# Kernel optimization log

Hardware: AMD Instinct MI355X
Metric: run time of the kernel (lower is better)

Reference implementation:

```python
import jax, jax.numpy as jnp
import numpy as np

EPS = 1e-12  # matches torch F.normalize eps default scale behavior (1e-12)

def _l2_normalize(x):
    n = jnp.sqrt(jnp.sum(x * x, axis=-1, keepdims=True))
    return x / jnp.maximum(n, EPS)

def setup_inputs() -> dict:
    key = jax.random.key(0)
    k1, k2 = jax.random.split(key)
    B, K, D = 32768, 4096, 1024
    context_repr = jax.random.normal(k1, (B, D), dtype=jnp.float32)
    # matches nn.init.normal_(std=0.02)
    cluster_centers = 0.02 * jax.random.normal(k2, (K, D), dtype=jnp.float32)
    return {"context_repr": context_repr, "cluster_centers": cluster_centers}

def reference(context_repr, cluster_centers):
    # L2-normalize rows of both
    x = _l2_normalize(context_repr)        # [B, D]
    c = _l2_normalize(cluster_centers)     # [K, D]
    x2 = jnp.sum(x * x, axis=-1, keepdims=True)          # [B, 1]
    c2 = jnp.sum(c * c, axis=-1)[None, :]                # [1, K]
    d2 = x2 + c2 - 2.0 * jnp.einsum('bd,kd->bk', x, c)   # [B, K]
    hard = jnp.argmin(d2, axis=-1)                       # [B]
    # Gather the UN-normalized learnable centers (as in the torch code)
    cluster_embedding = cluster_centers[hard]            # [B, D]
    return cluster_embedding
```

## Files before the change

### kernel.cpp

```cpp
#include <hip/hip_runtime.h>
#include <stdint.h>

#define B_ROWS 32768
#define K_CENT 4096
#define D_DIM  1024
#define EPS_CAND 5e-4f

typedef unsigned short u16;
typedef __attribute__((ext_vector_type(8))) __bf16 bf16x8;
typedef __attribute__((ext_vector_type(4))) float f32x4;

__device__ inline u16 f32_to_bf16(float f) {
    unsigned u = __float_as_uint(f);
    u += 0x7FFFu + ((u >> 16) & 1u);
    return (u16)(u >> 16);
}
__device__ inline float bf16_to_f32(u16 h) {
    return __uint_as_float(((unsigned)h) << 16);
}
__device__ inline unsigned ord_of_f32(float f) {
    unsigned u = __float_as_uint(f);
    return (u & 0x80000000u) ? ~u : (u | 0x80000000u);
}
__device__ inline float f32_of_ord(unsigned o) {
    unsigned u = (o & 0x80000000u) ? (o & 0x7fffffffu) : ~o;
    return __uint_as_float(u);
}

__global__ __launch_bounds__(256) void prep_rows(
    const float* __restrict__ src, u16* __restrict__ hi, u16* __restrict__ lo,
    float* __restrict__ sq, float* __restrict__ den)
{
    __shared__ double sm[4];
    const int row = blockIdx.x, tid = threadIdx.x;
    const float4 v = reinterpret_cast<const float4*>(src + (size_t)row * D_DIM)[tid];
    double ss = (double)v.x * v.x + (double)v.y * v.y
              + (double)v.z * v.z + (double)v.w * v.w;
#pragma unroll
    for (int m = 1; m < 64; m <<= 1) ss += __shfl_xor(ss, m, 64);
    if ((tid & 63) == 0) sm[tid >> 6] = ss;
    __syncthreads();
    const double tot = sm[0] + sm[1] + sm[2] + sm[3];
    const float d = fmaxf(sqrtf((float)tot), 1e-12f);
    const float n0 = v.x / d, n1 = v.y / d, n2 = v.z / d, n3 = v.w / d;

    ushort4 h, l;
    h.x = f32_to_bf16(n0); l.x = f32_to_bf16(n0 - bf16_to_f32(h.x));
    h.y = f32_to_bf16(n1); l.y = f32_to_bf16(n1 - bf16_to_f32(h.y));
    h.z = f32_to_bf16(n2); l.z = f32_to_bf16(n2 - bf16_to_f32(h.z));
    h.w = f32_to_bf16(n3); l.w = f32_to_bf16(n3 - bf16_to_f32(h.w));
    reinterpret_cast<ushort4*>(hi + (size_t)row * D_DIM)[tid] = h;
    reinterpret_cast<ushort4*>(lo + (size_t)row * D_DIM)[tid] = l;

    double s2 = (double)n0 * n0 + (double)n1 * n1
              + (double)n2 * n2 + (double)n3 * n3;
#pragma unroll
    for (int m = 1; m < 64; m <<= 1) s2 += __shfl_xor(s2, m, 64);
    __syncthreads();
    if ((tid & 63) == 0) sm[tid >> 6] = s2;
    __syncthreads();
    if (tid == 0) {
        sq[row] = (float)(sm[0] + sm[1] + sm[2] + sm[3]);
        den[row] = d;
    }
}

#define BM 256
#define BN 128
#define BK 32
#define NT (D_DIM / BK)
#define REG_U16 4096
#define TILE_U16 (6 * REG_U16)

__global__ __launch_bounds__(512, 2) void gemm_cand(
    const u16* __restrict__ Ahi, const u16* __restrict__ Alo,
    const u16* __restrict__ Bhi, const u16* __restrict__ Blo,
    const float* __restrict__ c2, unsigned long long* __restrict__ cand)
{
    __shared__ u16 lds[3 * TILE_U16];

    const int tid = threadIdx.x, lane = tid & 63, w = tid >> 6;
    const int wm = w >> 1, wn = w & 1;
    const int fr = lane & 15, fc = lane >> 4;

    const int flat = blockIdx.x;
    const int swz = (flat & 7) * 512 + (flat >> 3);
    int bx = swz & 31;
    const int by = swz >> 5;
    if (by & 1) bx = 31 - bx;
    const size_t arow0 = (size_t)by * BM;
    const size_t brow0 = (size_t)bx * BN;

    const int p = w * 64 + lane;
    const int srow = p >> 2;
    const int scc = (p & 3) ^ ((srow >> 1) & 3);
    const u16* gsrc[6];
    gsrc[0] = Ahi + (arow0 + srow) * D_DIM + scc * 8;
    gsrc[1] = Ahi + (arow0 + 128 + srow) * D_DIM + scc * 8;
    gsrc[2] = Alo + (arow0 + srow) * D_DIM + scc * 8;
    gsrc[3] = Alo + (arow0 + 128 + srow) * D_DIM + scc * 8;
    gsrc[4] = Bhi + (brow0 + srow) * D_DIM + scc * 8;
    gsrc[5] = Blo + (brow0 + srow) * D_DIM + scc * 8;
    const int ldw = w * 512;

    int offA[4], offB[4];
#pragma unroll
    for (int i = 0; i < 4; ++i) {
        const int ar = wm * 64 + i * 16 + fr;
        const int rg = ar >> 7, rr = ar & 127;
        offA[i] = rg * REG_U16 + rr * 32 + ((fc ^ ((rr >> 1) & 3)) * 8);
        const int br = wn * 64 + i * 16 + fr;
        offB[i] = br * 32 + ((fc ^ ((br >> 1) & 3)) * 8);
    }

    f32x4 acc[4][4] = {};

#define STAGE3(t, J0)                                                         \
    do {                                                                      \
        const int _base = ((t) % 3) * TILE_U16;                               \
        const int _k = (t) * BK;                                              \
        _Pragma("unroll")                                                     \
        for (int _j = (J0); _j < (J0) + 3; ++_j)                              \
            __builtin_amdgcn_global_load_lds(                                 \
                (const __attribute__((address_space(1))) void*)(gsrc[_j] + _k), \
                (__attribute__((address_space(3))) void*)(lds + _base + _j * REG_U16 + ldw), \
                16, 0, 0);                                                    \
    } while (0)

    STAGE3(0, 0); STAGE3(0, 3);
    STAGE3(1, 0); STAGE3(1, 3);
    asm volatile("s_waitcnt vmcnt(6)" ::: "memory");
    __builtin_amdgcn_s_barrier();

    for (int t = 0; t < NT; ++t) {
        const int cb = (t % 3) * TILE_U16;

        bf16x8 bhf[4], blf[4], ah0[2], al0[2];
#pragma unroll
        for (int n = 0; n < 4; ++n) {
            bhf[n] = *reinterpret_cast<const bf16x8*>(lds + cb + 4 * REG_U16 + offB[n]);
            blf[n] = *reinterpret_cast<const bf16x8*>(lds + cb + 5 * REG_U16 + offB[n]);
        }
#pragma unroll
        for (int i = 0; i < 2; ++i) {
            ah0[i] = *reinterpret_cast<const bf16x8*>(lds + cb + offA[i]);
            al0[i] = *reinterpret_cast<const bf16x8*>(lds + cb + 2 * REG_U16 + offA[i]);
        }
        if (t + 2 < NT) STAGE3(t + 2, 0);
        __builtin_amdgcn_sched_barrier(0);
        __builtin_amdgcn_s_barrier();
        __builtin_amdgcn_s_setprio(1);
#pragma unroll
        for (int i = 0; i < 2; ++i)
#pragma unroll
            for (int n = 0; n < 4; ++n)
                acc[i][n] = __builtin_amdgcn_mfma_f32_16x16x32_bf16(ah0[i], bhf[n], acc[i][n], 0, 0, 0);
#pragma unroll
        for (int i = 0; i < 2; ++i)
#pragma unroll
            for (int n = 0; n < 4; ++n)
                acc[i][n] = __builtin_amdgcn_mfma_f32_16x16x32_bf16(ah0[i], blf[n], acc[i][n], 0, 0, 0);
#pragma unroll
        for (int i = 0; i < 2; ++i)
#pragma unroll
            for (int n = 0; n < 4; ++n)
                acc[i][n] = __builtin_amdgcn_mfma_f32_16x16x32_bf16(al0[i], bhf[n], acc[i][n], 0, 0, 0);
        __builtin_amdgcn_s_setprio(0);
        __builtin_amdgcn_s_barrier();

        bf16x8 ah1[2], al1[2];
#pragma unroll
        for (int i = 0; i < 2; ++i) {
            ah1[i] = *reinterpret_cast<const bf16x8*>(lds + cb + offA[2 + i]);
            al1[i] = *reinterpret_cast<const bf16x8*>(lds + cb + 2 * REG_U16 + offA[2 + i]);
        }
        if (t + 2 < NT) STAGE3(t + 2, 3);
        __builtin_amdgcn_sched_barrier(0);
        __builtin_amdgcn_s_barrier();
        __builtin_amdgcn_s_setprio(1);
#pragma unroll
        for (int i = 0; i < 2; ++i)
#pragma unroll
            for (int n = 0; n < 4; ++n)
                acc[2 + i][n] = __builtin_amdgcn_mfma_f32_16x16x32_bf16(ah1[i], bhf[n], acc[2 + i][n], 0, 0, 0);
#pragma unroll
        for (int i = 0; i < 2; ++i)
#pragma unroll
            for (int n = 0; n < 4; ++n)
                acc[2 + i][n] = __builtin_amdgcn_mfma_f32_16x16x32_bf16(ah1[i], blf[n], acc[2 + i][n], 0, 0, 0);
#pragma unroll
        for (int i = 0; i < 2; ++i)
#pragma unroll
            for (int n = 0; n < 4; ++n)
                acc[2 + i][n] = __builtin_amdgcn_mfma_f32_16x16x32_bf16(al1[i], bhf[n], acc[2 + i][n], 0, 0, 0);
        __builtin_amdgcn_s_setprio(0);

        if (t < NT - 2)       asm volatile("s_waitcnt vmcnt(6)" ::: "memory");
        else if (t == NT - 2) asm volatile("s_waitcnt vmcnt(0)" ::: "memory");
        if (t < NT - 1) __builtin_amdgcn_s_barrier();
    }
#undef STAGE3

    const int group = bx * 2 + wn;
    float c2v[4];
#pragma unroll
    for (int n = 0; n < 4; ++n)
        c2v[n] = c2[brow0 + wn * 64 + n * 16 + fr];

#pragma unroll
    for (int mi = 0; mi < 4; ++mi) {
#pragma unroll
        for (int r = 0; r < 4; ++r) {
            unsigned long long bk = ~0ull;
#pragma unroll
            for (int ni = 0; ni < 4; ++ni) {
                const float d2a = c2v[ni] - 2.0f * acc[mi][ni][r];
                const unsigned col = (unsigned)(brow0 + wn * 64 + ni * 16 + fr);
                const unsigned long long key =
                    ((unsigned long long)ord_of_f32(d2a) << 32) | col;
                if (key < bk) bk = key;
            }
#pragma unroll
            for (int ms = 1; ms < 16; ms <<= 1) {
                const unsigned long long o = __shfl_xor(bk, ms, 64);
                if (o < bk) bk = o;
            }
            if (fr == 0) {
                const size_t grow = arow0 + wm * 64 + mi * 16 + fc * 4 + r;
                cand[grow * 64 + group] = bk;
            }
        }
    }
}

__global__ __launch_bounds__(256) void finalize(
    const unsigned long long* __restrict__ cand,
    const float* __restrict__ X, const float* __restrict__ C,
    const float* __restrict__ denx, const float* __restrict__ denc,
    const float* __restrict__ x2, const float* __restrict__ c2,
    float* __restrict__ out)
{
    const int w = threadIdx.x >> 6, lane = threadIdx.x & 63;
    const size_t row = (size_t)blockIdx.x * 4 + w;

    const unsigned long long v = cand[row * 64 + lane];
    unsigned long long m = v;
#pragma unroll
    for (int ms = 1; ms < 64; ms <<= 1) {
        const unsigned long long o = __shfl_xor(m, ms, 64);
        if (o < m) m = o;
    }
    const float fmin = f32_of_ord((unsigned)(m >> 32));
    const bool is_cand = f32_of_ord((unsigned)(v >> 32)) <= fmin + EPS_CAND;
    const unsigned long long ball = __ballot(is_cand);

    unsigned win;
    if (__popcll(ball) == 1) {
        win = (unsigned)(m & 0xffffffffu);
    } else {
        const float dxr = denx[row];
        const float x2r = x2[row];
        float xv[16];
#pragma unroll
        for (int j = 0; j < 16; ++j)
            xv[j] = X[row * D_DIM + j * 64 + lane] / dxr;

        float bestd2 = __uint_as_float(0x7f800000u);
        unsigned bwin = 0xffffffffu;
        unsigned long long bb = ball;
        while (bb) {
            const int l = __ffsll((unsigned long long)bb) - 1;
            bb &= bb - 1;
            const unsigned col = (unsigned)(__shfl(v, l, 64) & 0xffffffffu);
            const float dcr = denc[col];
            double s = 0.0;
#pragma unroll
            for (int j = 0; j < 16; ++j) {
                const float cv = C[(size_t)col * D_DIM + j * 64 + lane] / dcr;
                s = fma((double)xv[j], (double)cv, s);
            }
#pragma unroll
            for (int ms = 1; ms < 64; ms <<= 1) s += __shfl_xor(s, ms, 64);
            const float dotf = (float)s;
            const float d2 = (x2r + c2[col]) - 2.0f * dotf;
            if (d2 < bestd2 || (d2 == bestd2 && col < bwin)) {
                bestd2 = d2; bwin = col;
            }
        }
        win = bwin;
    }

    const float4* s4 = reinterpret_cast<const float4*>(C + (size_t)win * D_DIM);
    float4* d4 = reinterpret_cast<float4*>(out + row * D_DIM);
#pragma unroll
    for (int t = 0; t < 4; ++t) d4[t * 64 + lane] = s4[t * 64 + lane];
}

extern "C" void kernel_launch(void* const* d_in, const int* in_sizes, int n_in,
                              void* d_out, int out_size, void* d_ws, size_t ws_size,
                              hipStream_t stream)
{
    (void)in_sizes; (void)n_in; (void)out_size; (void)ws_size;
    const float* X = (const float*)d_in[0];
    const float* C = (const float*)d_in[1];
    float* out = (float*)d_out;

    char* ws = (char*)d_ws;
    u16* Ahi = (u16*)ws;
    u16* Alo = Ahi + (size_t)B_ROWS * D_DIM;
    u16* Bhi = Alo + (size_t)B_ROWS * D_DIM;
    u16* Blo = Bhi + (size_t)K_CENT * D_DIM;
    unsigned long long* cand =
        (unsigned long long*)(Blo + (size_t)K_CENT * D_DIM);
    float* c2   = (float*)(cand + (size_t)B_ROWS * 64);
    float* x2   = c2 + K_CENT;
    float* denx = x2 + B_ROWS;
    float* denc = denx + B_ROWS;

    prep_rows<<<B_ROWS, 256, 0, stream>>>(X, Ahi, Alo, x2, denx);
    prep_rows<<<K_CENT, 256, 0, stream>>>(C, Bhi, Blo, c2, denc);
    gemm_cand<<<(B_ROWS / BM) * (K_CENT / BN), 512, 0, stream>>>(
        Ahi, Alo, Bhi, Blo, c2, cand);
    finalize<<<B_ROWS / 4, 256, 0, stream>>>(
        cand, X, C, denx, denc, x2, c2, out);
}
```

Measured before the change: 1.060 ms.

## Enlarge GEMM tile to 256x256 and stream split-bf16 terms as K-phases

Widens the candidate GEMM block tile from 256x128 to 256x256 with 8 waves laid out 2x4, so each wave holds an 8x4 accumulator array. The three hi/lo product terms are no longer computed as separate MFMA groups inside each K step. Instead the K loop runs 48 steps over a concatenated K axis of hi*hi, lo*hi and hi*lo segments, selected by the tile index. The pipeline also moves from triple to double buffering with BK=64. The aim is more MFMA work per loaded byte and fewer separate fragment loads, at the cost of more accumulator registers and a shallower prefetch depth.

```diff
diff --git a/kernel.cpp b/kernel.cpp
--- a/kernel.cpp
+++ b/kernel.cpp
@@ -25,6 +25,11 @@
 __device__ inline float f32_of_ord(unsigned o) {
     unsigned u = (o & 0x80000000u) ? (o & 0x7fffffffu) : ~o;
     return __uint_as_float(u);
+}
+__device__ inline void gload_lds16(const u16* g, u16* l) {
+    __builtin_amdgcn_global_load_lds(
+        (const __attribute__((address_space(1))) void*)g,
+        (__attribute__((address_space(3))) void*)l, 16, 0, 0);
 }
 
 __global__ __launch_bounds__(256) void prep_rows(
@@ -66,149 +71,175 @@
 }
 
 #define BM 256
-#define BN 128
-#define BK 32
-#define NT (D_DIM / BK)
-#define REG_U16 4096
-#define TILE_U16 (6 * REG_U16)
+#define BN 256
+#define BK 64
+#define NT 48
+#define AREG 8192
+#define BOFF_U16 16384
+#define BUF_U16 32768
 
 __global__ __launch_bounds__(512, 2) void gemm_cand(
     const u16* __restrict__ Ahi, const u16* __restrict__ Alo,
     const u16* __restrict__ Bhi, const u16* __restrict__ Blo,
     const float* __restrict__ c2, unsigned long long* __restrict__ cand)
 {
-    __shared__ u16 lds[3 * TILE_U16];
+    __shared__ u16 lds[2 * BUF_U16];
 
     const int tid = threadIdx.x, lane = tid & 63, w = tid >> 6;
-    const int wm = w >> 1, wn = w & 1;
+    const int wm = w >> 2, wn = w & 3;
     const int fr = lane & 15, fc = lane >> 4;
 
     const int flat = blockIdx.x;
-    const int swz = (flat & 7) * 512 + (flat >> 3);
-    int bx = swz & 31;
-    const int by = swz >> 5;
-    if (by & 1) bx = 31 - bx;
+    const int swz = (flat & 7) * 256 + (flat >> 3);
+    int bx = swz & 15;
+    const int by = swz >> 4;
+    if (by & 1) bx = 15 - bx;
     const size_t arow0 = (size_t)by * BM;
     const size_t brow0 = (size_t)bx * BN;
 
-    const int p = w * 64 + lane;
-    const int srow = p >> 2;
-    const int scc = (p & 3) ^ ((srow >> 1) & 3);
-    const u16* gsrc[6];
-    gsrc[0] = Ahi + (arow0 + srow) * D_DIM + scc * 8;
-    gsrc[1] = Ahi + (arow0 + 128 + srow) * D_DIM + scc * 8;
-    gsrc[2] = Alo + (arow0 + srow) * D_DIM + scc * 8;
-    gsrc[3] = Alo + (arow0 + 128 + srow) * D_DIM + scc * 8;
-    gsrc[4] = Bhi + (brow0 + srow) * D_DIM + scc * 8;
-    gsrc[5] = Blo + (brow0 + srow) * D_DIM + scc * 8;
-    const int ldw = w * 512;
-
-    int offA[4], offB[4];
-#pragma unroll
-    for (int i = 0; i < 4; ++i) {
-        const int ar = wm * 64 + i * 16 + fr;
-        const int rg = ar >> 7, rr = ar & 127;
-        offA[i] = rg * REG_U16 + rr * 32 + ((fc ^ ((rr >> 1) & 3)) * 8);
-        const int br = wn * 64 + i * 16 + fr;
-        offB[i] = br * 32 + ((fc ^ ((br >> 1) & 3)) * 8);
-    }
-
-    f32x4 acc[4][4] = {};
-
-#define STAGE3(t, J0)                                                         \
-    do {                                                                      \
-        const int _base = ((t) % 3) * TILE_U16;                               \
-        const int _k = (t) * BK;                                              \
-        _Pragma("unroll")                                                     \
-        for (int _j = (J0); _j < (J0) + 3; ++_j)                              \
-            __builtin_amdgcn_global_load_lds(                                 \
-                (const __attribute__((address_space(1))) void*)(gsrc[_j] + _k), \
-                (__attribute__((address_space(3))) void*)(lds + _base + _j * REG_U16 + ldw), \
-                16, 0, 0);                                                    \
-    } while (0)
-
-    STAGE3(0, 0); STAGE3(0, 3);
-    STAGE3(1, 0); STAGE3(1, 3);
-    asm volatile("s_waitcnt vmcnt(6)" ::: "memory");
+    const int prow = tid >> 2, pch = tid & 3;
+    const int lc = pch ^ ((prow >> 1) & 3);
+    const size_t lane0 = (size_t)prow * D_DIM + lc * 8;
+    const size_t lane1 = (size_t)(prow + 128) * D_DIM + lc * 8;
+    const int dst0 = tid * 8, dst1 = tid * 8 + 4096;
+    const size_t abase = arow0 * D_DIM;
+    const size_t bbase = brow0 * D_DIM;
+
+#define STAGE_A(tn, jj) do {                                                  \
+    const u16* s_ = ((((tn) >> 4) == 1) ? Alo : Ahi) + abase                  \
+                    + ((size_t)((tn) & 15)) * BK + (jj) * 32;                 \
+    u16* d_ = lds + ((tn) & 1) * BUF_U16 + (jj) * AREG;                       \
+    gload_lds16(s_ + lane0, d_ + dst0);                                       \
+    gload_lds16(s_ + lane1, d_ + dst1);                                       \
+} while (0)
+#define STAGE_B(tn, jj) do {                                                  \
+    const u16* s_ = ((((tn) >> 4) == 2) ? Blo : Bhi) + bbase                  \
+                    + ((size_t)((tn) & 15)) * BK + (jj) * 32;                 \
+    u16* d_ = lds + ((tn) & 1) * BUF_U16 + BOFF_U16 + (jj) * AREG;            \
+    gload_lds16(s_ + lane0, d_ + dst0);                                       \
+    gload_lds16(s_ + lane1, d_ + dst1);                                       \
+} while (0)
+
+    int offA[8], offB[4];
+#pragma unroll
+    for (int i = 0; i < 8; ++i) {
+        const int r = wm * 128 + i * 16 + fr;
+        offA[i] = r * 32 + ((fc ^ ((r >> 1) & 3)) * 8);
+    }
+#pragma unroll
+    for (int n = 0; n < 4; ++n) {
+        const int r = wn * 64 + n * 16 + fr;
+        offB[n] = r * 32 + ((fc ^ ((r >> 1) & 3)) * 8);
+    }
+
+    f32x4 acc[8][4] = {};
+
+    STAGE_A(0, 0); STAGE_B(0, 0); STAGE_A(0, 1); STAGE_B(0, 1);
+    asm volatile("s_waitcnt vmcnt(4)" ::: "memory");
     __builtin_amdgcn_s_barrier();
+    __builtin_amdgcn_sched_barrier(0);
 
     for (int t = 0; t < NT; ++t) {
-        const int cb = (t % 3) * TILE_U16;
-
-        bf16x8 bhf[4], blf[4], ah0[2], al0[2];
-#pragma unroll
-        for (int n = 0; n < 4; ++n) {
-            bhf[n] = *reinterpret_cast<const bf16x8*>(lds + cb + 4 * REG_U16 + offB[n]);
-            blf[n] = *reinterpret_cast<const bf16x8*>(lds + cb + 5 * REG_U16 + offB[n]);
-        }
-#pragma unroll
-        for (int i = 0; i < 2; ++i) {
-            ah0[i] = *reinterpret_cast<const bf16x8*>(lds + cb + offA[i]);
-            al0[i] = *reinterpret_cast<const bf16x8*>(lds + cb + 2 * REG_U16 + offA[i]);
-        }
-        if (t + 2 < NT) STAGE3(t + 2, 0);
-        __builtin_amdgcn_sched_barrier(0);
-        __builtin_amdgcn_s_barrier();
+        const int cb = (t & 1) * BUF_U16;
+        const u16* LA = lds + cb;
+        const u16* LB = lds + cb + BOFF_U16;
+        const int tn = t + 1;
+        const bool st = tn < NT;
+
+        bf16x8 af[4], bfr[4];
+
+#pragma unroll
+        for (int n = 0; n < 4; ++n)
+            bfr[n] = *reinterpret_cast<const bf16x8*>(LB + offB[n]);
+#pragma unroll
+        for (int i = 0; i < 4; ++i)
+            af[i] = *reinterpret_cast<const bf16x8*>(LA + offA[i]);
+        if (st) STAGE_A(tn, 0);
+        __builtin_amdgcn_sched_barrier(0);
+        __builtin_amdgcn_s_barrier();
+        __builtin_amdgcn_sched_barrier(0);
         __builtin_amdgcn_s_setprio(1);
 #pragma unroll
-        for (int i = 0; i < 2; ++i)
+        for (int i = 0; i < 4; ++i)
 #pragma unroll
             for (int n = 0; n < 4; ++n)
-                acc[i][n] = __builtin_amdgcn_mfma_f32_16x16x32_bf16(ah0[i], bhf[n], acc[i][n], 0, 0, 0);
-#pragma unroll
-        for (int i = 0; i < 2; ++i)
+                acc[i][n] = __builtin_amdgcn_mfma_f32_16x16x32_bf16(af[i], bfr[n], acc[i][n], 0, 0, 0);
+        __builtin_amdgcn_s_setprio(0);
+        __builtin_amdgcn_sched_barrier(0);
+        __builtin_amdgcn_s_barrier();
+        __builtin_amdgcn_sched_barrier(0);
+
+#pragma unroll
+        for (int i = 0; i < 4; ++i)
+            af[i] = *reinterpret_cast<const bf16x8*>(LA + offA[4 + i]);
+        if (st) STAGE_B(tn, 0);
+        __builtin_amdgcn_sched_barrier(0);
+        __builtin_amdgcn_s_barrier();
+        __builtin_amdgcn_sched_barrier(0);
+        __builtin_amdgcn_s_setprio(1);
+#pragma unroll
+        for (int i = 0; i < 4; ++i)
 #pragma unroll
             for (int n = 0; n < 4; ++n)
-                acc[i][n] = __builtin_amdgcn_mfma_f32_16x16x32_bf16(ah0[i], blf[n], acc[i][n], 0, 0, 0);
-#pragma unroll
-        for (int i = 0; i < 2; ++i)
+                acc[4 + i][n] = __builtin_amdgcn_mfma_f32_16x16x32_bf16(af[i], bfr[n], acc[4 + i][n], 0, 0, 0);
+        __builtin_amdgcn_s_setprio(0);
+        if (t == NT - 1) asm volatile("s_waitcnt vmcnt(0)" ::: "memory");
+        else             asm volatile("s_waitcnt vmcnt(4)" ::: "memory");
+        __builtin_amdgcn_sched_barrier(0);
+        __builtin_amdgcn_s_barrier();
+        __builtin_amdgcn_sched_barrier(0);
+
+#pragma unroll
+        for (int n = 0; n < 4; ++n)
+            bfr[n] = *reinterpret_cast<const bf16x8*>(LB + AREG + offB[n]);
+#pragma unroll
+        for (int i = 0; i < 4; ++i)
+            af[i] = *reinterpret_cast<const bf16x8*>(LA + AREG + offA[i]);
+        if (st) STAGE_A(tn, 1);
+        __builtin_amdgcn_sched_barrier(0);
+        __builtin_amdgcn_s_barrier();
+        __builtin_amdgcn_sched_barrier(0);
+        __builtin_amdgcn_s_setprio(1);
+#pragma unroll
+        for (int i = 0; i < 4; ++i)
 #pragma unroll
             for (int n = 0; n < 4; ++n)
-                acc[i][n] = __builtin_amdgcn_mfma_f32_16x16x32_bf16(al0[i], bhf[n], acc[i][n], 0, 0, 0);
+                acc[i][n] = __builtin_amdgcn_mfma_f32_16x16x32_bf16(af[i], bfr[n], acc[i][n], 0, 0, 0);
         __builtin_amdgcn_s_setprio(0);
-        __builtin_amdgcn_s_barrier();
-
-        bf16x8 ah1[2], al1[2];
-#pragma unroll
-        for (int i = 0; i < 2; ++i) {
-            ah1[i] = *reinterpret_cast<const bf16x8*>(lds + cb + offA[2 + i]);
-            al1[i] = *reinterpret_cast<const bf16x8*>(lds + cb + 2 * REG_U16 + offA[2 + i]);
-        }
-        if (t + 2 < NT) STAGE3(t + 2, 3);
-        __builtin_amdgcn_sched_barrier(0);
-        __builtin_amdgcn_s_barrier();
+        __builtin_amdgcn_sched_barrier(0);
+        __builtin_amdgcn_s_barrier();
+        __builtin_amdgcn_sched_barrier(0);
+
+#pragma unroll
+        for (int i = 0; i < 4; ++i)
+            af[i] = *reinterpret_cast<const bf16x8*>(LA + AREG + offA[4 + i]);
+        if (st) STAGE_B(tn, 1);
+        __builtin_amdgcn_sched_barrier(0);
+        __builtin_amdgcn_s_barrier();
+        __builtin_amdgcn_sched_barrier(0);
         __builtin_amdgcn_s_setprio(1);
 #pragma unroll
-        for (int i = 0; i < 2; ++i)
+        for (int i = 0; i < 4; ++i)
 #pragma unroll
             for (int n = 0; n < 4; ++n)
-                acc[2 + i][n] = __builtin_amdgcn_mfma_f32_16x16x32_bf16(ah1[i], bhf[n], acc[2 + i][n], 0, 0, 0);
-#pragma unroll
-        for (int i = 0; i < 2; ++i)
-#pragma unroll
-            for (int n = 0; n < 4; ++n)
-                acc[2 + i][n] = __builtin_amdgcn_mfma_f32_16x16x32_bf16(ah1[i], blf[n], acc[2 + i][n], 0, 0, 0);
-#pragma unroll
-        for (int i = 0; i < 2; ++i)
-#pragma unroll
-            for (int n = 0; n < 4; ++n)
-                acc[2 + i][n] = __builtin_amdgcn_mfma_f32_16x16x32_bf16(al1[i], bhf[n], acc[2 + i][n], 0, 0, 0);
+                acc[4 + i][n] = __builtin_amdgcn_mfma_f32_16x16x32_bf16(af[i], bfr[n], acc[4 + i][n], 0, 0, 0);
         __builtin_amdgcn_s_setprio(0);
-
-        if (t < NT - 2)       asm volatile("s_waitcnt vmcnt(6)" ::: "memory");
-        else if (t == NT - 2) asm volatile("s_waitcnt vmcnt(0)" ::: "memory");
-        if (t < NT - 1) __builtin_amdgcn_s_barrier();
-    }
-#undef STAGE3
-
-    const int group = bx * 2 + wn;
+        if (t < NT - 1) asm volatile("s_waitcnt vmcnt(4)" ::: "memory");
+        __builtin_amdgcn_sched_barrier(0);
+        __builtin_amdgcn_s_barrier();
+        __builtin_amdgcn_sched_barrier(0);
+    }
+#undef STAGE_A
+#undef STAGE_B
+
+    const int group = bx * 4 + wn;
     float c2v[4];
 #pragma unroll
     for (int n = 0; n < 4; ++n)
         c2v[n] = c2[brow0 + wn * 64 + n * 16 + fr];
 
 #pragma unroll
-    for (int mi = 0; mi < 4; ++mi) {
+    for (int mi = 0; mi < 8; ++mi) {
 #pragma unroll
         for (int r = 0; r < 4; ++r) {
             unsigned long long bk = ~0ull;
@@ -226,7 +257,7 @@
                 if (o < bk) bk = o;
             }
             if (fr == 0) {
-                const size_t grow = arow0 + wm * 64 + mi * 16 + fc * 4 + r;
+                const size_t grow = arow0 + wm * 128 + mi * 16 + fc * 4 + r;
                 cand[grow * 64 + group] = bk;
             }
         }
```

Result: faster. 990.8 us (-6.6%).
